# Optimization experiments

Measured on AMD Instinct MI355X. Metric: run time of the kernel, lower is better.

Reference implementation:

```python
import jax, jax.numpy as jnp
import numpy as np

B, H, K = 4096, 256, 16
INPUT_DIM, XPRIME_DIM = 8, 64
D = INPUT_DIM * XPRIME_DIM  # 512
LN_EPS = 1e-5


def setup_inputs() -> dict:
    key = jax.random.key(0)
    ks = jax.random.split(key, 12)
    s1 = 1.0  # Linear(1, D): fan_in=1
    sD = 1.0 / np.sqrt(D)
    sH = 1.0 / np.sqrt(H)
    return {
        "h_prev_rnn": jax.random.normal(ks[0], (B, H), jnp.float32),
        "x_l": jax.random.normal(ks[1], (B, INPUT_DIM), jnp.float32),
        "x_ext": jax.random.normal(ks[2], (B, K), jnp.float32),
        # stacked per-expert MetaNet params
        "meta_w1": jax.random.uniform(ks[3], (K, D), jnp.float32, -s1, s1),
        "meta_b1": jax.random.uniform(ks[4], (K, D), jnp.float32, -s1, s1),
        "meta_w2": jax.random.uniform(ks[5], (K, D, D), jnp.float32, -sD, sD),
        "meta_b2": jax.random.uniform(ks[6], (K, D), jnp.float32, -sD, sD),
        # gating net
        "gw1": jax.random.uniform(ks[7], (H, H), jnp.float32, -sH, sH),
        "gb1": jax.random.uniform(ks[8], (H,), jnp.float32, -sH, sH),
        "gw2": jax.random.uniform(ks[9], (H, K), jnp.float32, -sH, sH),
        "gb2": jax.random.uniform(ks[10], (K,), jnp.float32, -sH, sH),
        # LayerNorm([input_dim, xprime_dim]) affine params
        "ln_g": jnp.ones((INPUT_DIM, XPRIME_DIM), jnp.float32),
        "ln_b": jnp.zeros((INPUT_DIM, XPRIME_DIM), jnp.float32),
        "theta0": jnp.zeros((1, INPUT_DIM, XPRIME_DIM), jnp.float32),
    }


def reference(h_prev_rnn, x_l, x_ext, meta_w1, meta_b1, meta_w2, meta_b2,
              gw1, gb1, gw2, gb2, ln_g, ln_b, theta0):
    # MetaNet layer1 (Linear(1, D)): scalar input per expert -> [B, K, D]
    h1 = jnp.tanh(x_ext[:, :, None] * meta_w1[None] + meta_b1[None])
    # MetaNet layer2: per-expert DxD GEMM
    h2 = jnp.tanh(jnp.einsum('bkd,kde->bke', h1, meta_w2) + meta_b2[None])
    W = h2.reshape(h2.shape[0], K, INPUT_DIM, XPRIME_DIM)  # [B,K,i,e]
    # LayerNorm over last two dims jointly, affine
    mu = W.mean(axis=(-2, -1), keepdims=True)
    var = W.var(axis=(-2, -1), keepdims=True)
    W = (W - mu) * jax.lax.rsqrt(var + LN_EPS) * ln_g + ln_b
    # gating: softmax over experts (epoch/top_k = None path)
    logits = jnp.tanh(h_prev_rnn @ gw1 + gb1) @ gw2 + gb2
    gates = jax.nn.softmax(logits, axis=-1)  # [B, K]
    theta = jnp.einsum('bk,bkie->bie', gates, W) + theta0  # [B, i, e]
    x_prime = jnp.einsum('bi,bie->be', x_l, theta)  # [B, e]
    return (x_prime, theta)
```

## Files before the change

kernel.cpp:

```cpp
#include <hip/hip_runtime.h>
#include <hip/hip_bf16.h>
#include <stdint.h>

#define NB   4096
#define NH   256
#define NK   16
#define ND   512

using short8  = __attribute__((ext_vector_type(8))) short;
using float4v = __attribute__((ext_vector_type(4))) float;
typedef unsigned short ushort;

__device__ __forceinline__ float fast_tanh(float x) {
  float e = __builtin_amdgcn_exp2f(x * 2.88539008177793f);
  return 1.0f - 2.0f * __builtin_amdgcn_rcpf(e + 1.0f);
}

__device__ __forceinline__ ushort f2bf(float f) {
  union { float f; unsigned u; } v; v.f = f;
  unsigned r = v.u + 0x7FFF + ((v.u >> 16) & 1);
  return (ushort)(r >> 16);
}

__device__ __forceinline__ float bf2f(ushort h) {
  union { unsigned u; float f; } v; v.u = ((unsigned)h) << 16; return v.f;
}

__device__ __forceinline__ unsigned pk2(float a, float b) {
  __hip_bfloat162 h = __float22bfloat162_rn(float2{a, b});
  unsigned u; __builtin_memcpy(&u, &h, 4); return u;
}

__global__ __launch_bounds__(256) void k_prep(
    const float* __restrict__ w2, const float* __restrict__ h_prev,
    const float* __restrict__ gw1, const float* __restrict__ gb1,
    const float* __restrict__ gw2, const float* __restrict__ gb2,
    ushort* __restrict__ B2, float* __restrict__ gates) {
  __shared__ float sbuf[4160];
  const int t = threadIdx.x;
  const int lin = blockIdx.x;

  if (lin < 1024) {
    const int w = lin;
    const int e0 = (w & 7) * 64;
    const int d0 = ((w >> 3) & 7) * 64;
    const int k = w >> 6;
    float (*sh)[65] = (float(*)[65])sbuf;
    const float* src = w2 + ((size_t)k * ND + d0) * ND + e0;
#pragma unroll
    for (int rep = 0; rep < 4; ++rep) {
      int r = rep * 16 + (t >> 4);
      int c = (t & 15) * 4;
      float4 v = *(const float4*)&src[(size_t)r * ND + c];
      sh[r][c] = v.x; sh[r][c + 1] = v.y; sh[r][c + 2] = v.z; sh[r][c + 3] = v.w;
    }
    __syncthreads();
#pragma unroll
    for (int s = 0; s < 2; ++s) {
      int idx = t + s * 256;
      int kh = idx >> 8;
      int rem = idx & 255;
      int e = e0 + (rem >> 2);
      int c8 = (rem & 3) * 8;
      int kk = (d0 >> 5) + kh;
      ushort o[8];
#pragma unroll
      for (int j = 0; j < 8; ++j) o[j] = f2bf(sh[kh * 32 + c8 + j][e - e0]);
      *(uint4*)&B2[(((size_t)(k * 16 + kk)) * ND + e) * 32 + c8] = *(uint4*)o;
    }
  } else {
    const int b0 = (lin - 1024) * 8;
    float* sh_h = sbuf;
    float* sh_t = sbuf + 2048;
    for (int r = 0; r < 8; ++r) sh_h[r * 256 + t] = h_prev[(b0 + r) * NH + t];
    __syncthreads();
    float acc[8];
    float bias = gb1[t];
#pragma unroll
    for (int r = 0; r < 8; ++r) acc[r] = bias;
    for (int i = 0; i < NH; i += 4) {
      float w0 = gw1[(i + 0) * NH + t];
      float w1v = gw1[(i + 1) * NH + t];
      float w2v = gw1[(i + 2) * NH + t];
      float w3 = gw1[(i + 3) * NH + t];
#pragma unroll
      for (int r = 0; r < 8; ++r) {
        float4 hv = *(const float4*)&sh_h[r * 256 + i];
        acc[r] += hv.x * w0 + hv.y * w1v + hv.z * w2v + hv.w * w3;
      }
    }
#pragma unroll
    for (int r = 0; r < 8; ++r) sh_t[t * 8 + r] = fast_tanh(acc[r]);
    __syncthreads();
    if (t < 128) {
      const int r = t >> 4, k = t & 15;
      float lg = gb2[k];
      for (int j = 0; j < NH; ++j) lg += sh_t[j * 8 + r] * gw2[j * NK + k];
      float m = lg;
      for (int off = 1; off < 16; off <<= 1) m = fmaxf(m, __shfl_xor(m, off, 16));
      float e = __builtin_amdgcn_exp2f((lg - m) * 1.44269504f);
      float s = e;
      for (int off = 1; off < 16; off <<= 1) s += __shfl_xor(s, off, 16);
      gates[(b0 + r) * NK + k] = e * __builtin_amdgcn_rcpf(s);
    }
  }
}

__global__ __launch_bounds__(256, 2) void k_gemm(
    const float* __restrict__ x_ext, const float* __restrict__ w1,
    const float* __restrict__ b1,
    const ushort* __restrict__ B2,
    const float* __restrict__ b2,
    ushort* __restrict__ h2raw) {
  __shared__ __align__(16) ushort smem[16 * 64 * 36];
  ushort* sA = smem;
  ushort* tp = smem;

  const int t = threadIdx.x;
  const int l = t & 63, w = t >> 6;
  const int wn = w;
  const int q = l >> 4, m16 = l & 15;

  const int lin = blockIdx.x;
  const int xcd = lin & 7;
  const int slot = lin >> 3;
  const int ke = xcd * 2 + (slot >> 6);
  const int m0 = (slot & 63) * 64;

  const ushort* Bbase =
      B2 + ((size_t)(ke * 16)) * (ND * 32) + (wn * 128 + m16) * 32 + q * 8;
  short8 bf[2][8];
  auto loadB = [&](int kk, int slotr) {
#pragma unroll
    for (int bni = 0; bni < 8; ++bni)
      bf[slotr][bni] = *(const short8*)(Bbase + (size_t)kk * (ND * 32) + bni * 512);
  };
  loadB(0, 0);
  loadB(1, 1);

  {
    const int r = t >> 2, ac8 = (t & 3) * 8;
    const float x = x_ext[(m0 + r) * NK + ke];
    const float* w1k = w1 + ke * ND;
    const float* b1k = b1 + ke * ND;
#pragma unroll
    for (int kk = 0; kk < 16; ++kk) {
      const int d = kk * 32 + ac8;
      float4 wlo = *(const float4*)&w1k[d];
      float4 whi = *(const float4*)&w1k[d + 4];
      float4 blo = *(const float4*)&b1k[d];
      float4 bhi = *(const float4*)&b1k[d + 4];
      unsigned o4[4];
      o4[0] = pk2(fast_tanh(x * wlo.x + blo.x), fast_tanh(x * wlo.y + blo.y));
      o4[1] = pk2(fast_tanh(x * wlo.z + blo.z), fast_tanh(x * wlo.w + blo.w));
      o4[2] = pk2(fast_tanh(x * whi.x + bhi.x), fast_tanh(x * whi.y + bhi.y));
      o4[3] = pk2(fast_tanh(x * whi.z + bhi.z), fast_tanh(x * whi.w + bhi.w));
      *(uint4*)&sA[kk * 2304 + r * 36 + ac8] = *(uint4*)o4;
    }
  }
  __syncthreads();

  float4v acc[4][8];
#pragma unroll
  for (int f = 0; f < 4; ++f)
#pragma unroll
    for (int bni = 0; bni < 8; ++bni) acc[f][bni] = (float4v){0.f, 0.f, 0.f, 0.f};

#pragma unroll
  for (int kk = 0; kk < 16; ++kk) {
    const int cur = kk & 1;
    short8 af[4];
#pragma unroll
    for (int f = 0; f < 4; ++f)
      af[f] = *(const short8*)&sA[kk * 2304 + (f * 16 + m16) * 36 + q * 8];
#pragma unroll
    for (int f = 0; f < 4; ++f)
#pragma unroll
      for (int bni = 0; bni < 8; ++bni)
        acc[f][bni] = __builtin_amdgcn_mfma_f32_16x16x32_bf16(
            af[f], bf[cur][bni], acc[f][bni], 0, 0, 0);
    if (kk < 14) loadB(kk + 2, cur);
  }
  __syncthreads();

  {
    float b2v[8];
#pragma unroll
    for (int bni = 0; bni < 8; ++bni)
      b2v[bni] = b2[ke * ND + wn * 128 + bni * 16 + m16];
#pragma unroll
    for (int f = 0; f < 4; ++f)
#pragma unroll
      for (int rr = 0; rr < 4; ++rr) {
        int row = f * 16 + q * 4 + rr;
#pragma unroll
        for (int bni = 0; bni < 8; ++bni)
          tp[row * 524 + wn * 128 + bni * 16 + m16] =
              f2bf(fast_tanh(acc[f][bni][rr] + b2v[bni]));
      }
  }
  __syncthreads();
#pragma unroll
  for (int it = 0; it < 16; ++it) {
    int idx = it * 256 + t;
    int row = idx >> 6;
    int c8 = (idx & 63) * 8;
    *(uint4*)&h2raw[((size_t)(m0 + row) * NK + ke) * ND + c8] =
        *(uint4*)&tp[row * 524 + c8];
  }
}

__global__ __launch_bounds__(256) void k_final(
    const ushort* __restrict__ h2raw,
    const float* __restrict__ gates,
    const float* __restrict__ x_l,
    const float* __restrict__ ln_g, const float* __restrict__ ln_b,
    const float* __restrict__ theta0,
    float* __restrict__ out) {
  const int t = threadIdx.x;
  const int l = t & 63;
  const int b = blockIdx.x * 4 + (t >> 6);
  const int d0 = l * 8;
  const ushort* P = h2raw + (size_t)b * NK * ND + d0;
  uint4 raw[16];
#pragma unroll
  for (int k = 0; k < NK; ++k) raw[k] = *(const uint4*)&P[k * ND];
  float g[8], bb[8], acc[8];
  *(float4*)&g[0] = *(const float4*)&ln_g[d0];
  *(float4*)&g[4] = *(const float4*)&ln_g[d0 + 4];
  *(float4*)&bb[0] = *(const float4*)&ln_b[d0];
  *(float4*)&bb[4] = *(const float4*)&ln_b[d0 + 4];
#pragma unroll
  for (int j = 0; j < 8; ++j) acc[j] = 0.f;
#pragma unroll
  for (int k = 0; k < NK; ++k) {
    const ushort* hp = (const ushort*)&raw[k];
    float v[8];
#pragma unroll
    for (int j = 0; j < 8; ++j) v[j] = bf2f(hp[j]);
    float s = 0.f, s2 = 0.f;
#pragma unroll
    for (int j = 0; j < 8; ++j) { s += v[j]; s2 += v[j] * v[j]; }
#pragma unroll
    for (int off = 1; off < 64; off <<= 1) {
      s += __shfl_xor(s, off, 64);
      s2 += __shfl_xor(s2, off, 64);
    }
    float mu = s * (1.f / 512.f);
    float var = s2 * (1.f / 512.f) - mu * mu;
    float rs = __builtin_amdgcn_rsqf(var + 1e-5f);
    float gate = gates[b * NK + k];
    float a = gate * rs;
#pragma unroll
    for (int j = 0; j < 8; ++j)
      acc[j] += a * g[j] * (v[j] - mu) + gate * bb[j];
  }
  float th[8];
  *(float4*)&th[0] = *(const float4*)&theta0[d0];
  *(float4*)&th[4] = *(const float4*)&theta0[d0 + 4];
#pragma unroll
  for (int j = 0; j < 8; ++j) th[j] += acc[j];
  float* thp = out + (size_t)NB * 64 + (size_t)b * ND + d0;
  *(float4*)&thp[0] = *(float4*)&th[0];
  *(float4*)&thp[4] = *(float4*)&th[4];
  const float xl = x_l[b * 8 + (l >> 3)];
  float p[8];
#pragma unroll
  for (int j = 0; j < 8; ++j) p[j] = xl * th[j];
  for (int off = 8; off < 64; off <<= 1)
#pragma unroll
    for (int j = 0; j < 8; ++j) p[j] += __shfl_xor(p[j], off, 64);
  if (l < 8) {
    float* xp = out + (size_t)b * 64 + l * 8;
    *(float4*)&xp[0] = *(float4*)&p[0];
    *(float4*)&xp[4] = *(float4*)&p[4];
  }
}

extern "C" void kernel_launch(void* const* d_in, const int* in_sizes, int n_in,
                              void* d_out, int out_size, void* d_ws, size_t ws_size,
                              hipStream_t stream) {
  const float* h_prev = (const float*)d_in[0];
  const float* x_l    = (const float*)d_in[1];
  const float* x_ext  = (const float*)d_in[2];
  const float* mw1    = (const float*)d_in[3];
  const float* mb1    = (const float*)d_in[4];
  const float* mw2    = (const float*)d_in[5];
  const float* mb2    = (const float*)d_in[6];
  const float* gw1    = (const float*)d_in[7];
  const float* gb1    = (const float*)d_in[8];
  const float* gw2    = (const float*)d_in[9];
  const float* gb2    = (const float*)d_in[10];
  const float* ln_g   = (const float*)d_in[11];
  const float* ln_b   = (const float*)d_in[12];
  const float* th0    = (const float*)d_in[13];
  float* out = (float*)d_out;

  char* ws = (char*)d_ws;
  float* gates = (float*)ws;
  ushort* B2    = (ushort*)(ws + (1u << 18));
  ushort* h2raw = (ushort*)(ws + (1u << 18) + (16u << 20));

  hipLaunchKernelGGL(k_prep, dim3(1536), dim3(256), 0, stream,
                     mw2, h_prev, gw1, gb1, gw2, gb2, B2, gates);
  hipLaunchKernelGGL(k_gemm, dim3(1024), dim3(256), 0, stream,
                     x_ext, mw1, mb1, B2, mb2, h2raw);
  hipLaunchKernelGGL(k_final, dim3(NB / 4), dim3(256), 0, stream,
                     h2raw, gates, x_l, ln_g, ln_b, th0, out);
}
```

Before: 193.0 us.

## Halve GEMM LDS footprint via two-phase A generation to raise occupancy

The A tile (tanh of the layer-1 activations) is now generated in two halves of 8 K-steps instead of all 16 at once. The output transpose staging is likewise split into two 32-row passes. Together these halve shared memory per block, which allows raising launch bounds from 2 to 4 blocks per CU so all GEMM blocks can be resident together. The cost is extra barriers between phases and tighter register limits, which risk spills given the large MFMA accumulator and B-prefetch arrays.

```diff
diff --git a/kernel.cpp b/kernel.cpp
--- a/kernel.cpp
+++ b/kernel.cpp
@@ -106,13 +106,13 @@
   }
 }
 
-__global__ __launch_bounds__(256, 2) void k_gemm(
+__global__ __launch_bounds__(256, 4) void k_gemm(
     const float* __restrict__ x_ext, const float* __restrict__ w1,
     const float* __restrict__ b1,
     const ushort* __restrict__ B2,
     const float* __restrict__ b2,
     ushort* __restrict__ h2raw) {
-  __shared__ __align__(16) ushort smem[16 * 64 * 36];
+  __shared__ __align__(16) ushort smem[8 * 64 * 36];
   ushort* sA = smem;
   ushort* tp = smem;
 
@@ -138,26 +138,28 @@
   loadB(0, 0);
   loadB(1, 1);
 
-  {
-    const int r = t >> 2, ac8 = (t & 3) * 8;
-    const float x = x_ext[(m0 + r) * NK + ke];
-    const float* w1k = w1 + ke * ND;
-    const float* b1k = b1 + ke * ND;
-#pragma unroll
-    for (int kk = 0; kk < 16; ++kk) {
-      const int d = kk * 32 + ac8;
+  const int r = t >> 2, ac8 = (t & 3) * 8;
+  const float xval = x_ext[(m0 + r) * NK + ke];
+  const float* w1k = w1 + ke * ND;
+  const float* b1k = b1 + ke * ND;
+  auto genA = [&](int h) {
+#pragma unroll
+    for (int kkl = 0; kkl < 8; ++kkl) {
+      const int d = (h * 8 + kkl) * 32 + ac8;
       float4 wlo = *(const float4*)&w1k[d];
       float4 whi = *(const float4*)&w1k[d + 4];
       float4 blo = *(const float4*)&b1k[d];
       float4 bhi = *(const float4*)&b1k[d + 4];
       unsigned o4[4];
-      o4[0] = pk2(fast_tanh(x * wlo.x + blo.x), fast_tanh(x * wlo.y + blo.y));
-      o4[1] = pk2(fast_tanh(x * wlo.z + blo.z), fast_tanh(x * wlo.w + blo.w));
-      o4[2] = pk2(fast_tanh(x * whi.x + bhi.x), fast_tanh(x * whi.y + bhi.y));
-      o4[3] = pk2(fast_tanh(x * whi.z + bhi.z), fast_tanh(x * whi.w + bhi.w));
-      *(uint4*)&sA[kk * 2304 + r * 36 + ac8] = *(uint4*)o4;
-    }
-  }
+      o4[0] = pk2(fast_tanh(xval * wlo.x + blo.x), fast_tanh(xval * wlo.y + blo.y));
+      o4[1] = pk2(fast_tanh(xval * wlo.z + blo.z), fast_tanh(xval * wlo.w + blo.w));
+      o4[2] = pk2(fast_tanh(xval * whi.x + bhi.x), fast_tanh(xval * whi.y + bhi.y));
+      o4[3] = pk2(fast_tanh(xval * whi.z + bhi.z), fast_tanh(xval * whi.w + bhi.w));
+      *(uint4*)&sA[kkl * 2304 + r * 36 + ac8] = *(uint4*)o4;
+    }
+  };
+
+  genA(0);
   __syncthreads();
 
   float4v acc[4][8];
@@ -167,46 +169,59 @@
     for (int bni = 0; bni < 8; ++bni) acc[f][bni] = (float4v){0.f, 0.f, 0.f, 0.f};
 
 #pragma unroll
-  for (int kk = 0; kk < 16; ++kk) {
-    const int cur = kk & 1;
-    short8 af[4];
-#pragma unroll
-    for (int f = 0; f < 4; ++f)
-      af[f] = *(const short8*)&sA[kk * 2304 + (f * 16 + m16) * 36 + q * 8];
-#pragma unroll
-    for (int f = 0; f < 4; ++f)
-#pragma unroll
-      for (int bni = 0; bni < 8; ++bni)
-        acc[f][bni] = __builtin_amdgcn_mfma_f32_16x16x32_bf16(
-            af[f], bf[cur][bni], acc[f][bni], 0, 0, 0);
-    if (kk < 14) loadB(kk + 2, cur);
+  for (int h = 0; h < 2; ++h) {
+    if (h == 1) {
+      __syncthreads();
+      genA(1);
+      __syncthreads();
+    }
+#pragma unroll
+    for (int kkl = 0; kkl < 8; ++kkl) {
+      const int kk = h * 8 + kkl;
+      short8 af[4];
+#pragma unroll
+      for (int f = 0; f < 4; ++f)
+        af[f] = *(const short8*)&sA[kkl * 2304 + (f * 16 + m16) * 36 + q * 8];
+#pragma unroll
+      for (int f = 0; f < 4; ++f)
+#pragma unroll
+        for (int bni = 0; bni < 8; ++bni)
+          acc[f][bni] = __builtin_amdgcn_mfma_f32_16x16x32_bf16(
+              af[f], bf[kk & 1][bni], acc[f][bni], 0, 0, 0);
+      if (kk < 14) loadB(kk + 2, kk & 1);
+    }
   }
   __syncthreads();
 
-  {
-    float b2v[8];
-#pragma unroll
-    for (int bni = 0; bni < 8; ++bni)
-      b2v[bni] = b2[ke * ND + wn * 128 + bni * 16 + m16];
-#pragma unroll
-    for (int f = 0; f < 4; ++f)
+  float b2v[8];
+#pragma unroll
+  for (int bni = 0; bni < 8; ++bni)
+    b2v[bni] = b2[ke * ND + wn * 128 + bni * 16 + m16];
+
+#pragma unroll
+  for (int p = 0; p < 2; ++p) {
+#pragma unroll
+    for (int fl = 0; fl < 2; ++fl) {
+      int f = p * 2 + fl;
 #pragma unroll
       for (int rr = 0; rr < 4; ++rr) {
-        int row = f * 16 + q * 4 + rr;
+        int row_local = fl * 16 + q * 4 + rr;
 #pragma unroll
         for (int bni = 0; bni < 8; ++bni)
-          tp[row * 524 + wn * 128 + bni * 16 + m16] =
+          tp[row_local * 524 + wn * 128 + bni * 16 + m16] =
               f2bf(fast_tanh(acc[f][bni][rr] + b2v[bni]));
       }
-  }
-  __syncthreads();
-#pragma unroll
-  for (int it = 0; it < 16; ++it) {
-    int idx = it * 256 + t;
-    int row = idx >> 6;
-    int c8 = (idx & 63) * 8;
-    *(uint4*)&h2raw[((size_t)(m0 + row) * NK + ke) * ND + c8] =
-        *(uint4*)&tp[row * 524 + c8];
+    }
+    __syncthreads();
+#pragma unroll
+    for (int it = 0; it < 8; ++it) {
+      int idx = it * 256 + t;
+      int row = idx >> 6;
+      int c8 = (idx & 63) * 8;
+      *(uint4*)&h2raw[((size_t)(m0 + p * 32 + row) * NK + ke) * ND + c8] =
+          *(uint4*)&tp[row * 524 + c8];
+    }
+    if (p == 0) __syncthreads();
   }
 }
 
```

New measurement: 433.9 us. 125% more time.

## Fuse LayerNorm and gate reduction into GEMM epilogue over expert groups

Applied to the files above, without the earlier changes.

The GEMM kernel now loops over four experts per block and applies tanh, LayerNorm statistics, gating and the affine transform in registers. It accumulates a partial theta per expert group and writes it in fp32, so the large bf16 per-expert activation buffer is no longer written and reread. The final kernel only sums the four partials, adds theta0 and computes x_prime. The trade-off is a grid of 256 blocks at one block per CU, which lowers occupancy and leaves more B-tile loads exposed. There are also extra syncs for the cross-wave row statistics.

```diff
diff --git a/kernel.cpp b/kernel.cpp
--- a/kernel.cpp
+++ b/kernel.cpp
@@ -20,10 +20,6 @@
   union { float f; unsigned u; } v; v.f = f;
   unsigned r = v.u + 0x7FFF + ((v.u >> 16) & 1);
   return (ushort)(r >> 16);
-}
-
-__device__ __forceinline__ float bf2f(ushort h) {
-  union { unsigned u; float f; } v; v.u = ((unsigned)h) << 16; return v.f;
 }
 
 __device__ __forceinline__ unsigned pk2(float a, float b) {
@@ -106,160 +102,190 @@
   }
 }
 
-__global__ __launch_bounds__(256, 2) void k_gemm(
+__global__ __launch_bounds__(256, 1) void k_gemm(
     const float* __restrict__ x_ext, const float* __restrict__ w1,
     const float* __restrict__ b1,
     const ushort* __restrict__ B2,
     const float* __restrict__ b2,
-    ushort* __restrict__ h2raw) {
-  __shared__ __align__(16) ushort smem[16 * 64 * 36];
-  ushort* sA = smem;
-  ushort* tp = smem;
+    const float* __restrict__ gates,
+    const float* __restrict__ ln_g, const float* __restrict__ ln_b,
+    float* __restrict__ tpart) {
+  __shared__ __align__(16) ushort sA[16 * 64 * 36];
+  __shared__ float ps[4][64][2];
+  __shared__ __align__(16) float fin[64][4];
 
   const int t = threadIdx.x;
-  const int l = t & 63, w = t >> 6;
-  const int wn = w;
+  const int l = t & 63, wn = t >> 6;
   const int q = l >> 4, m16 = l & 15;
 
   const int lin = blockIdx.x;
   const int xcd = lin & 7;
-  const int slot = lin >> 3;
-  const int ke = xcd * 2 + (slot >> 6);
-  const int m0 = (slot & 63) * 64;
-
-  const ushort* Bbase =
-      B2 + ((size_t)(ke * 16)) * (ND * 32) + (wn * 128 + m16) * 32 + q * 8;
-  short8 bf[2][8];
-  auto loadB = [&](int kk, int slotr) {
+  const int eq = xcd >> 1;
+  const int m0 = ((lin >> 3) * 2 + (xcd & 1)) * 64;
+
+  float gld[8], lbd[8];
+#pragma unroll
+  for (int bni = 0; bni < 8; ++bni) {
+    int n = wn * 128 + bni * 16 + m16;
+    gld[bni] = ln_g[n];
+    lbd[bni] = ln_b[n];
+  }
+
+  float th[4][8][4];
+#pragma unroll
+  for (int f = 0; f < 4; ++f)
 #pragma unroll
     for (int bni = 0; bni < 8; ++bni)
-      bf[slotr][bni] = *(const short8*)(Bbase + (size_t)kk * (ND * 32) + bni * 512);
-  };
-  loadB(0, 0);
-  loadB(1, 1);
-
-  {
-    const int r = t >> 2, ac8 = (t & 3) * 8;
-    const float x = x_ext[(m0 + r) * NK + ke];
-    const float* w1k = w1 + ke * ND;
-    const float* b1k = b1 + ke * ND;
+#pragma unroll
+      for (int rr = 0; rr < 4; ++rr) th[f][bni][rr] = 0.f;
+
+  const int ar = t >> 2, ac8 = (t & 3) * 8;
+
+  for (int ei = 0; ei < 4; ++ei) {
+    const int ke = eq * 4 + ei;
+
+    {
+      const float x = x_ext[(m0 + ar) * NK + ke];
+      const float* w1k = w1 + ke * ND;
+      const float* b1k = b1 + ke * ND;
+#pragma unroll
+      for (int kk = 0; kk < 16; ++kk) {
+        const int d = kk * 32 + ac8;
+        float4 wlo = *(const float4*)&w1k[d];
+        float4 whi = *(const float4*)&w1k[d + 4];
+        float4 blo = *(const float4*)&b1k[d];
+        float4 bhi = *(const float4*)&b1k[d + 4];
+        unsigned o4[4];
+        o4[0] = pk2(fast_tanh(x * wlo.x + blo.x), fast_tanh(x * wlo.y + blo.y));
+        o4[1] = pk2(fast_tanh(x * wlo.z + blo.z), fast_tanh(x * wlo.w + blo.w));
+        o4[2] = pk2(fast_tanh(x * whi.x + bhi.x), fast_tanh(x * whi.y + bhi.y));
+        o4[3] = pk2(fast_tanh(x * whi.z + bhi.z), fast_tanh(x * whi.w + bhi.w));
+        *(uint4*)&sA[kk * 2304 + ar * 36 + ac8] = *(uint4*)o4;
+      }
+    }
+    __syncthreads();
+
+    const ushort* Bbase =
+        B2 + ((size_t)(ke * 16)) * (ND * 32) + (wn * 128 + m16) * 32 + q * 8;
+    short8 bf[2][8];
+    auto loadB = [&](int kk, int slotr) {
+#pragma unroll
+      for (int bni = 0; bni < 8; ++bni)
+        bf[slotr][bni] = *(const short8*)(Bbase + (size_t)kk * (ND * 32) + bni * 512);
+    };
+    loadB(0, 0);
+    loadB(1, 1);
+
+    float4v acc[4][8];
+#pragma unroll
+    for (int f = 0; f < 4; ++f)
+#pragma unroll
+      for (int bni = 0; bni < 8; ++bni) acc[f][bni] = (float4v){0.f, 0.f, 0.f, 0.f};
+
 #pragma unroll
     for (int kk = 0; kk < 16; ++kk) {
-      const int d = kk * 32 + ac8;
-      float4 wlo = *(const float4*)&w1k[d];
-      float4 whi = *(const float4*)&w1k[d + 4];
-      float4 blo = *(const float4*)&b1k[d];
-      float4 bhi = *(const float4*)&b1k[d + 4];
-      unsigned o4[4];
-      o4[0] = pk2(fast_tanh(x * wlo.x + blo.x), fast_tanh(x * wlo.y + blo.y));
-      o4[1] = pk2(fast_tanh(x * wlo.z + blo.z), fast_tanh(x * wlo.w + blo.w));
-      o4[2] = pk2(fast_tanh(x * whi.x + bhi.x), fast_tanh(x * whi.y + bhi.y));
-      o4[3] = pk2(fast_tanh(x * whi.z + bhi.z), fast_tanh(x * whi.w + bhi.w));
-      *(uint4*)&sA[kk * 2304 + r * 36 + ac8] = *(uint4*)o4;
-    }
-  }
-  __syncthreads();
-
-  float4v acc[4][8];
-#pragma unroll
-  for (int f = 0; f < 4; ++f)
-#pragma unroll
-    for (int bni = 0; bni < 8; ++bni) acc[f][bni] = (float4v){0.f, 0.f, 0.f, 0.f};
-
-#pragma unroll
-  for (int kk = 0; kk < 16; ++kk) {
-    const int cur = kk & 1;
-    short8 af[4];
+      short8 af[4];
+#pragma unroll
+      for (int f = 0; f < 4; ++f)
+        af[f] = *(const short8*)&sA[kk * 2304 + (f * 16 + m16) * 36 + q * 8];
+#pragma unroll
+      for (int f = 0; f < 4; ++f)
+#pragma unroll
+        for (int bni = 0; bni < 8; ++bni)
+          acc[f][bni] = __builtin_amdgcn_mfma_f32_16x16x32_bf16(
+              af[f], bf[kk & 1][bni], acc[f][bni], 0, 0, 0);
+      if (kk < 14) loadB(kk + 2, kk & 1);
+    }
+
+    {
+      float b2v[8];
+#pragma unroll
+      for (int bni = 0; bni < 8; ++bni)
+        b2v[bni] = b2[ke * ND + wn * 128 + bni * 16 + m16];
+#pragma unroll
+      for (int f = 0; f < 4; ++f)
+#pragma unroll
+        for (int bni = 0; bni < 8; ++bni)
+#pragma unroll
+          for (int rr = 0; rr < 4; ++rr)
+            acc[f][bni][rr] = fast_tanh(acc[f][bni][rr] + b2v[bni]);
+    }
 #pragma unroll
     for (int f = 0; f < 4; ++f)
-      af[f] = *(const short8*)&sA[kk * 2304 + (f * 16 + m16) * 36 + q * 8];
-#pragma unroll
-    for (int f = 0; f < 4; ++f)
-#pragma unroll
-      for (int bni = 0; bni < 8; ++bni)
-        acc[f][bni] = __builtin_amdgcn_mfma_f32_16x16x32_bf16(
-            af[f], bf[cur][bni], acc[f][bni], 0, 0, 0);
-    if (kk < 14) loadB(kk + 2, cur);
-  }
-  __syncthreads();
-
-  {
-    float b2v[8];
-#pragma unroll
-    for (int bni = 0; bni < 8; ++bni)
-      b2v[bni] = b2[ke * ND + wn * 128 + bni * 16 + m16];
+#pragma unroll
+      for (int rr = 0; rr < 4; ++rr) {
+        float s = 0.f, s2 = 0.f;
+#pragma unroll
+        for (int bni = 0; bni < 8; ++bni) {
+          float v = acc[f][bni][rr];
+          s += v; s2 += v * v;
+        }
+#pragma unroll
+        for (int off = 1; off < 16; off <<= 1) {
+          s += __shfl_xor(s, off, 64);
+          s2 += __shfl_xor(s2, off, 64);
+        }
+        if (m16 == 0) {
+          int row = f * 16 + q * 4 + rr;
+          *(float2*)&ps[wn][row][0] = (float2){s, s2};
+        }
+      }
+    __syncthreads();
+    if (t < 64) {
+      float s  = ps[0][t][0] + ps[1][t][0] + ps[2][t][0] + ps[3][t][0];
+      float s2 = ps[0][t][1] + ps[1][t][1] + ps[2][t][1] + ps[3][t][1];
+      float mu = s * (1.f / 512.f);
+      float var = s2 * (1.f / 512.f) - mu * mu;
+      float rs = __builtin_amdgcn_rsqf(var + 1e-5f);
+      float gate = gates[(m0 + t) * NK + ke];
+      fin[t][0] = mu; fin[t][1] = gate * rs; fin[t][2] = gate; fin[t][3] = 0.f;
+    }
+    __syncthreads();
 #pragma unroll
     for (int f = 0; f < 4; ++f)
 #pragma unroll
       for (int rr = 0; rr < 4; ++rr) {
         int row = f * 16 + q * 4 + rr;
+        float4 fr = *(float4*)&fin[row][0];
 #pragma unroll
         for (int bni = 0; bni < 8; ++bni)
-          tp[row * 524 + wn * 128 + bni * 16 + m16] =
-              f2bf(fast_tanh(acc[f][bni][rr] + b2v[bni]));
+          th[f][bni][rr] += fr.y * gld[bni] * (acc[f][bni][rr] - fr.x) + fr.z * lbd[bni];
       }
-  }
-  __syncthreads();
-#pragma unroll
-  for (int it = 0; it < 16; ++it) {
-    int idx = it * 256 + t;
-    int row = idx >> 6;
-    int c8 = (idx & 63) * 8;
-    *(uint4*)&h2raw[((size_t)(m0 + row) * NK + ke) * ND + c8] =
-        *(uint4*)&tp[row * 524 + c8];
-  }
+    __syncthreads();
+  }
+
+  float* dst = tpart + (size_t)eq * NB * ND;
+#pragma unroll
+  for (int f = 0; f < 4; ++f)
+#pragma unroll
+    for (int rr = 0; rr < 4; ++rr) {
+      int row = m0 + f * 16 + q * 4 + rr;
+#pragma unroll
+      for (int bni = 0; bni < 8; ++bni)
+        dst[(size_t)row * ND + wn * 128 + bni * 16 + m16] = th[f][bni][rr];
+    }
 }
 
 __global__ __launch_bounds__(256) void k_final(
-    const ushort* __restrict__ h2raw,
-    const float* __restrict__ gates,
+    const float* __restrict__ tpart,
     const float* __restrict__ x_l,
-    const float* __restrict__ ln_g, const float* __restrict__ ln_b,
     const float* __restrict__ theta0,
     float* __restrict__ out) {
   const int t = threadIdx.x;
   const int l = t & 63;
   const int b = blockIdx.x * 4 + (t >> 6);
   const int d0 = l * 8;
-  const ushort* P = h2raw + (size_t)b * NK * ND + d0;
-  uint4 raw[16];
-#pragma unroll
-  for (int k = 0; k < NK; ++k) raw[k] = *(const uint4*)&P[k * ND];
-  float g[8], bb[8], acc[8];
-  *(float4*)&g[0] = *(const float4*)&ln_g[d0];
-  *(float4*)&g[4] = *(const float4*)&ln_g[d0 + 4];
-  *(float4*)&bb[0] = *(const float4*)&ln_b[d0];
-  *(float4*)&bb[4] = *(const float4*)&ln_b[d0 + 4];
-#pragma unroll
-  for (int j = 0; j < 8; ++j) acc[j] = 0.f;
-#pragma unroll
-  for (int k = 0; k < NK; ++k) {
-    const ushort* hp = (const ushort*)&raw[k];
-    float v[8];
-#pragma unroll
-    for (int j = 0; j < 8; ++j) v[j] = bf2f(hp[j]);
-    float s = 0.f, s2 = 0.f;
-#pragma unroll
-    for (int j = 0; j < 8; ++j) { s += v[j]; s2 += v[j] * v[j]; }
-#pragma unroll
-    for (int off = 1; off < 64; off <<= 1) {
-      s += __shfl_xor(s, off, 64);
-      s2 += __shfl_xor(s2, off, 64);
-    }
-    float mu = s * (1.f / 512.f);
-    float var = s2 * (1.f / 512.f) - mu * mu;
-    float rs = __builtin_amdgcn_rsqf(var + 1e-5f);
-    float gate = gates[b * NK + k];
-    float a = gate * rs;
-#pragma unroll
-    for (int j = 0; j < 8; ++j)
-      acc[j] += a * g[j] * (v[j] - mu) + gate * bb[j];
-  }
   float th[8];
   *(float4*)&th[0] = *(const float4*)&theta0[d0];
   *(float4*)&th[4] = *(const float4*)&theta0[d0 + 4];
 #pragma unroll
-  for (int j = 0; j < 8; ++j) th[j] += acc[j];
+  for (int p = 0; p < 4; ++p) {
+    const float* P = tpart + ((size_t)p * NB + b) * ND + d0;
+    float4 a = *(const float4*)&P[0];
+    float4 c = *(const float4*)&P[4];
+    th[0] += a.x; th[1] += a.y; th[2] += a.z; th[3] += a.w;
+    th[4] += c.x; th[5] += c.y; th[6] += c.z; th[7] += c.w;
+  }
   float* thp = out + (size_t)NB * 64 + (size_t)b * ND + d0;
   *(float4*)&thp[0] = *(float4*)&th[0];
   *(float4*)&thp[4] = *(float4*)&th[4];
@@ -297,14 +323,14 @@
   float* out = (float*)d_out;
 
   char* ws = (char*)d_ws;
-  float* gates = (float*)ws;
+  float* gates  = (float*)ws;
   ushort* B2    = (ushort*)(ws + (1u << 18));
-  ushort* h2raw = (ushort*)(ws + (1u << 18) + (16u << 20));
+  float* tpart  = (float*)(ws + (1u << 18) + (16u << 20));
 
   hipLaunchKernelGGL(k_prep, dim3(1536), dim3(256), 0, stream,
                      mw2, h_prev, gw1, gb1, gw2, gb2, B2, gates);
-  hipLaunchKernelGGL(k_gemm, dim3(1024), dim3(256), 0, stream,
-                     x_ext, mw1, mb1, B2, mb2, h2raw);
+  hipLaunchKernelGGL(k_gemm, dim3(256), dim3(256), 0, stream,
+                     x_ext, mw1, mb1, B2, mb2, gates, ln_g, ln_b, tpart);
   hipLaunchKernelGGL(k_final, dim3(NB / 4), dim3(256), 0, stream,
-                     h2raw, gates, x_l, ln_g, ln_b, th0, out);
-}
+                     tpart, x_l, th0, out);
+}
```

Measured after the change: 230.8 us. 19.6% more time.
